# Performance work log

Hardware: AMD Instinct MI355X
Metric: run time of the kernel (lower is better)

## Reference

```python
import jax, jax.numpy as jnp
import numpy as np

N = 50000          # nodes
DEG = 16           # in-degree per node
E = N * DEG        # edges
HID = 128          # hidden_channels (x_channels)
NH = 32            # num_heads (hardcoded in StarPool)
HD = HID // NH     # head dim
ECH = 64           # edge channels = num_rbf + num_edge_attr
NG = 64            # number of graphs in batch
OUT = 1            # output_dim
EPS = 1e-5


def setup_inputs() -> dict:
    key = jax.random.key(0)
    ks = jax.random.split(key, 12)
    x = jax.random.normal(ks[0], (N, HID), jnp.float32)
    edge_attr = jax.random.normal(ks[1], (E, ECH), jnp.float32)
    # edge_index: row0 = source j (random), row1 = target i covering all nodes
    src = jax.random.randint(ks[2], (E,), 0, N, dtype=jnp.int32)
    dst = jnp.repeat(jnp.arange(N, dtype=jnp.int32), DEG)
    edge_index = jnp.stack([src, dst], axis=0)
    batch = jnp.sort(jax.random.randint(ks[3], (N,), 0, NG, dtype=jnp.int32))
    # learned parameters (xavier-ish scaling)
    s_h = 1.0 / np.sqrt(HID)
    s_e = 1.0 / np.sqrt(ECH)
    Wq = jax.random.normal(ks[4], (HID, HID), jnp.float32) * s_h
    bq = jnp.zeros((HID,), jnp.float32)
    Wkv = jax.random.normal(ks[5], (HID, HID), jnp.float32) * s_h
    bkv = jnp.zeros((HID,), jnp.float32)
    Wdk = jax.random.normal(ks[6], (ECH, HID), jnp.float32) * s_e
    bdk = jnp.zeros((HID,), jnp.float32)
    ln_in_g = jnp.ones((HID,), jnp.float32)
    ln_in_b = jnp.zeros((HID,), jnp.float32)
    ln_out_g = jnp.ones((HID,), jnp.float32)
    ln_out_b = jnp.zeros((HID,), jnp.float32)
    Wout = jax.random.normal(ks[7], (HID, OUT), jnp.float32) * s_h
    bout = jnp.zeros((OUT,), jnp.float32)
    return {"x": x, "edge_attr": edge_attr, "Wq": Wq, "bq": bq, "Wkv": Wkv,
            "bkv": bkv, "Wdk": Wdk, "bdk": bdk, "ln_in_g": ln_in_g,
            "ln_in_b": ln_in_b, "ln_out_g": ln_out_g, "ln_out_b": ln_out_b,
            "Wout": Wout, "bout": bout, "edge_index": edge_index, "batch": batch}


def _layernorm(z, g, b):
    m = jnp.mean(z, axis=-1, keepdims=True)
    v = jnp.mean(jnp.square(z - m), axis=-1, keepdims=True)
    return (z - m) * jax.lax.rsqrt(v + EPS) * g + b


def reference(x, edge_attr, Wq, bq, Wkv, bkv, Wdk, bdk,
              ln_in_g, ln_in_b, ln_out_g, ln_out_b, Wout, bout,
              edge_index, batch):
    n = x.shape[0]
    residue = x
    xn = _layernorm(x, ln_in_g, ln_in_b)
    q = (xn @ Wq + bq).reshape(n, NH, HD)
    k = (xn @ Wkv + bkv).reshape(n, NH, HD)          # v = k in StarPool
    dk = (edge_attr @ Wdk + bdk).reshape(-1, NH, HD)
    src, dst = edge_index[0], edge_index[1]          # j (source), i (target)
    k_j = k[src]                                     # [E, NH, HD]
    attn = jax.nn.silu(jnp.sum(q[dst] * k_j * dk, axis=-1))  # [E, NH]
    msg = k_j * attn[:, :, None]                     # [E, NH, HD]
    # scatter-mean over target nodes
    counts = jax.ops.segment_sum(jnp.ones((msg.shape[0],), x.dtype), dst, num_segments=n)
    agg = jax.ops.segment_sum(msg, dst, num_segments=n)
    agg = agg / jnp.clip(counts, 1.0)[:, None, None]
    h = residue + agg.reshape(n, HID)
    # perm = unique(edge_index[1]) == arange(n) by input construction (identity)
    h = residue + _layernorm(h, ln_out_g, ln_out_b)  # dropout p=0 -> identity
    # per-graph mean readout (reduce_op='mean')
    gcnt = jax.ops.segment_sum(jnp.ones((n,), x.dtype), batch, num_segments=NG)
    g = jax.ops.segment_sum(h, batch, num_segments=NG) / jnp.clip(gcnt, 1.0)[:, None]
    # output MLP with 'pass' (identity) activation
    return g @ Wout + bout
```

## Files before the change

### kernel.cpp

```cpp
#include <hip/hip_runtime.h>
#include <hip/hip_bf16.h>

#define N_NODES 50000
#define DEG 16
#define NE 800000
#define HID 128
#define NH 32
#define ECH 64
#define NG 64
#define NSLOT 32
#define LN_EPS 1e-5f

typedef __bf16 bf16x8 __attribute__((ext_vector_type(8)));
typedef float f32x4 __attribute__((ext_vector_type(4)));

__device__ __forceinline__ unsigned short f2bf(float f) {
  unsigned int u = __float_as_uint(f);
  u += 0x7FFFu + ((u >> 16) & 1u);
  return (unsigned short)(u >> 16);
}
__device__ __forceinline__ unsigned int pack2(float a, float b) {
  return (unsigned int)f2bf(a) | ((unsigned int)f2bf(b) << 16);
}

__global__ void prep_kernel(const float* __restrict__ Wq, const float* __restrict__ Wkv,
                            const float* __restrict__ Wdk,
                            unsigned short* __restrict__ WBf,
                            unsigned short* __restrict__ Wdkf,
                            float* __restrict__ gsum) {
  int b = blockIdx.x, t = threadIdx.x;
  if (b < 16) {
    int n = b;
    for (int idx = t; idx < 2048; idx += 256) {
      int j = idx & 7, l = (idx >> 3) & 63, kk = idx >> 9;
      int col = n * 16 + (l & 15);
      int k = kk * 32 + (l >> 4) * 8 + j;
      float v = (col < HID) ? Wq[k * HID + col] : Wkv[k * HID + (col - HID)];
      WBf[((n * 4 + kk) * 64 + l) * 8 + j] = f2bf(v);
    }
  } else if (b < 24) {
    int n2 = b - 16;
    for (int idx = t; idx < 1024; idx += 256) {
      int j = idx & 7, l = (idx >> 3) & 63, kk = idx >> 9;
      int col = n2 * 16 + (l & 15);
      int k = kk * 32 + (l >> 4) * 8 + j;
      Wdkf[((n2 * 2 + kk) * 64 + l) * 8 + j] = f2bf(Wdk[k * HID + col]);
    }
  } else {
    int chunk = b - 24;
    const int tot = NG * NSLOT * HID / 8;
    for (int i = chunk * tot + t; i < (chunk + 1) * tot; i += 256)
      gsum[i] = 0.0f;
  }
}

__global__ __launch_bounds__(256) void node_kernel(
    const float* __restrict__ x, const float* __restrict__ bq,
    const float* __restrict__ bkv, const float* __restrict__ lng,
    const float* __restrict__ lnb, const unsigned short* __restrict__ WBf,
    float* __restrict__ qout, unsigned short* __restrict__ kout) {
  __shared__ __align__(16) unsigned short xn[64 * HID];
  int t = threadIdx.x;
  int node0 = blockIdx.x * 64;
  {
    int row = t >> 2, q4 = t & 3;
    int c0 = q4 * 32;
    int node = node0 + row;
    float v[32];
    if (node < N_NODES) {
      const float4* xp = (const float4*)(x + node * HID + c0);
#pragma unroll
      for (int i = 0; i < 8; i++) {
        float4 f = xp[i];
        v[4 * i] = f.x; v[4 * i + 1] = f.y; v[4 * i + 2] = f.z; v[4 * i + 3] = f.w;
      }
    } else {
#pragma unroll
      for (int i = 0; i < 32; i++) v[i] = 0.f;
    }
    float s = 0.f;
#pragma unroll
    for (int i = 0; i < 32; i++) s += v[i];
    s += __shfl_xor(s, 1); s += __shfl_xor(s, 2);
    float m = s * (1.0f / HID);
    float sq = 0.f;
#pragma unroll
    for (int i = 0; i < 32; i++) { float d = v[i] - m; sq += d * d; }
    sq += __shfl_xor(sq, 1); sq += __shfl_xor(sq, 2);
    float rstd = rsqrtf(sq * (1.0f / HID) + LN_EPS);
#pragma unroll
    for (int ch = 0; ch < 4; ch++) {
      float w0[8];
#pragma unroll
      for (int j = 0; j < 8; j++) {
        int c = c0 + ch * 8 + j;
        w0[j] = (v[ch * 8 + j] - m) * rstd * lng[c] + lnb[c];
      }
      uint4 u;
      u.x = pack2(w0[0], w0[1]); u.y = pack2(w0[2], w0[3]);
      u.z = pack2(w0[4], w0[5]); u.w = pack2(w0[6], w0[7]);
      int byte = row * 256 + ((c0 * 2 + ch * 16) ^ ((row & 7) << 4));
      *(uint4*)((char*)xn + byte) = u;
    }
  }
  __syncthreads();
  int w = t >> 6, l = t & 63;
  int arow = w * 16 + (l & 15);
  bf16x8 a[4];
#pragma unroll
  for (int kk = 0; kk < 4; kk++) {
    int byte = arow * 256 + ((kk * 64 + (l >> 4) * 16) ^ ((arow & 7) << 4));
    a[kk] = *(const bf16x8*)((const char*)xn + byte);
  }
  f32x4 acc[16];
#pragma unroll
  for (int n = 0; n < 16; n++) acc[n] = (f32x4){0.f, 0.f, 0.f, 0.f};
#pragma unroll
  for (int n = 0; n < 16; n++)
#pragma unroll
    for (int kk = 0; kk < 4; kk++) {
      bf16x8 bfr = *(const bf16x8*)(WBf + ((n * 4 + kk) * 64 + l) * 8);
      acc[n] = __builtin_amdgcn_mfma_f32_16x16x32_bf16(a[kk], bfr, acc[n], 0, 0, 0);
    }
#pragma unroll
  for (int n = 0; n < 16; n++) {
    int col = n * 16 + (l & 15);
    float bias = (col < HID) ? bq[col] : bkv[col - HID];
#pragma unroll
    for (int r = 0; r < 4; r++) {
      int node = node0 + w * 16 + (l >> 4) * 4 + r;
      if (node < N_NODES) {
        float vv = acc[n][r] + bias;
        if (col < HID) qout[node * HID + col] = vv;
        else kout[node * HID + (col - HID)] = f2bf(vv);
      }
    }
  }
}

__global__ __launch_bounds__(256, 4) void edge_kernel(
    const float* __restrict__ x, const float* __restrict__ ea,
    const int* __restrict__ src_arr, const int* __restrict__ batch,
    const float* __restrict__ bdk, const float* __restrict__ lng,
    const float* __restrict__ lnb, const float* __restrict__ qg,
    const unsigned short* __restrict__ kbf,
    const unsigned short* __restrict__ Wdkf, float* __restrict__ gsum) {
  __shared__ __align__(16) float xq_s[8 * HID];
  __shared__ __align__(16) float prm_s[3 * HID];
  __shared__ __align__(16) float at_s[4 * 16 * 33];
  __shared__ __align__(16) float h_s[4 * 132];
  __shared__ __align__(16) unsigned short k_s[4 * 16 * HID];
  __shared__ int src_s[64];
  __shared__ int b4[4];
  int t = threadIdx.x;
  int node0 = blockIdx.x * 4;
  int w = t >> 6, l = t & 63, el = l & 15, eh = l >> 4;
  size_t e0n = (size_t)(node0 + w) * DEG;

  xq_s[t]       = x[(size_t)node0 * HID + t];
  xq_s[256 + t] = x[(size_t)node0 * HID + 256 + t];
  xq_s[512 + t] = qg[(size_t)node0 * HID + t];
  xq_s[768 + t] = qg[(size_t)node0 * HID + 256 + t];
  if (t < HID) { prm_s[t] = bdk[t]; prm_s[HID + t] = lng[t]; prm_s[2 * HID + t] = lnb[t]; }
  if (t < 64) src_s[t] = src_arr[(size_t)node0 * DEG + t];
  if (t < 4) b4[t] = batch[node0 + t];

  const float* earow = ea + (e0n + el) * ECH + eh * 8;
  f32x4 ea00 = __builtin_nontemporal_load((const f32x4*)(earow));
  f32x4 ea01 = __builtin_nontemporal_load((const f32x4*)(earow + 4));
  f32x4 ea10 = __builtin_nontemporal_load((const f32x4*)(earow + 32));
  f32x4 ea11 = __builtin_nontemporal_load((const f32x4*)(earow + 36));

  bf16x8 bfr[2];
  bfr[0][0] = (__bf16)ea00[0]; bfr[0][1] = (__bf16)ea00[1];
  bfr[0][2] = (__bf16)ea00[2]; bfr[0][3] = (__bf16)ea00[3];
  bfr[0][4] = (__bf16)ea01[0]; bfr[0][5] = (__bf16)ea01[1];
  bfr[0][6] = (__bf16)ea01[2]; bfr[0][7] = (__bf16)ea01[3];
  bfr[1][0] = (__bf16)ea10[0]; bfr[1][1] = (__bf16)ea10[1];
  bfr[1][2] = (__bf16)ea10[2]; bfr[1][3] = (__bf16)ea10[3];
  bfr[1][4] = (__bf16)ea11[0]; bfr[1][5] = (__bf16)ea11[1];
  bfr[1][6] = (__bf16)ea11[2]; bfr[1][7] = (__bf16)ea11[3];

  __syncthreads();

  unsigned int kw[16];
#pragma unroll
  for (int e = 0; e < 16; e++) {
    int sw = src_s[w * 16 + e];
    kw[e] = *(const unsigned int*)(kbf + (size_t)sw * HID + 2 * l);
  }
  char* kswW = (char*)k_s + w * 4096;
#pragma unroll
  for (int e = 0; e < 16; e++)
    *(unsigned int*)(kswW + e * 256 + ((4 * l) ^ ((e & 7) << 4))) = kw[e];

  f32x4 acc[8];
#pragma unroll
  for (int n = 0; n < 8; n++) acc[n] = (f32x4){0.f, 0.f, 0.f, 0.f};
#pragma unroll
  for (int n = 0; n < 8; n++)
#pragma unroll
    for (int kk = 0; kk < 2; kk++) {
      bf16x8 af = *(const bf16x8*)(Wdkf + ((n * 2 + kk) * 64 + l) * 8);
      acc[n] = __builtin_amdgcn_mfma_f32_16x16x32_bf16(af, bfr[kk], acc[n], 0, 0, 0);
    }

  const char* kswR = (const char*)k_s + w * 4096;
#pragma unroll
  for (int n = 0; n < 8; n++) {
    const int cb = n * 16 + eh * 4;
    f32x4 qv = *(const f32x4*)&xq_s[512 + w * HID + cb];
    f32x4 bd = *(const f32x4*)&prm_s[cb];
    uint2 kk2 = *(const uint2*)(kswR + el * 256 + ((n * 32 + eh * 8) ^ ((el & 7) << 4)));
    float k0 = __uint_as_float(kk2.x << 16);
    float k1 = __uint_as_float(kk2.x & 0xFFFF0000u);
    float k2 = __uint_as_float(kk2.y << 16);
    float k3 = __uint_as_float(kk2.y & 0xFFFF0000u);
    float d0 = acc[n][0] + bd[0];
    float d1 = acc[n][1] + bd[1];
    float d2 = acc[n][2] + bd[2];
    float d3 = acc[n][3] + bd[3];
    float s = qv[0] * k0 * d0 + qv[1] * k1 * d1 + qv[2] * k2 * d2 + qv[3] * k3 * d3;
    float at = s * __builtin_amdgcn_rcpf(1.0f + __expf(-s));
    at_s[w * 528 + el * 33 + n * 4 + eh] = at;
  }

  int hl = l >> 1;
  float macc0 = 0.f, macc1 = 0.f;
#pragma unroll
  for (int e = 0; e < 16; e++) {
    float at = at_s[w * 528 + e * 33 + hl];
    float k0 = __uint_as_float(kw[e] << 16);
    float k1 = __uint_as_float(kw[e] & 0xFFFF0000u);
    macc0 = fmaf(k0, at, macc0);
    macc1 = fmaf(k1, at, macc1);
  }
  float2 xv = *(const float2*)&xq_s[w * HID + 2 * l];
  float h10 = xv.x + macc0 * 0.0625f;
  float h11 = xv.y + macc1 * 0.0625f;
  float ss = h10 + h11;
  ss += __shfl_xor(ss, 1);  ss += __shfl_xor(ss, 2);  ss += __shfl_xor(ss, 4);
  ss += __shfl_xor(ss, 8);  ss += __shfl_xor(ss, 16); ss += __shfl_xor(ss, 32);
  float mean = ss * (1.0f / HID);
  float dv0 = h10 - mean, dv1 = h11 - mean;
  float vv = dv0 * dv0 + dv1 * dv1;
  vv += __shfl_xor(vv, 1);  vv += __shfl_xor(vv, 2);  vv += __shfl_xor(vv, 4);
  vv += __shfl_xor(vv, 8);  vv += __shfl_xor(vv, 16); vv += __shfl_xor(vv, 32);
  float rstd = rsqrtf(vv * (1.0f / HID) + LN_EPS);
  float2 gv = *(const float2*)&prm_s[HID + 2 * l];
  float2 bv = *(const float2*)&prm_s[2 * HID + 2 * l];
  float2 ho;
  ho.x = xv.x + dv0 * rstd * gv.x + bv.x;
  ho.y = xv.y + dv1 * rstd * gv.y + bv.y;
  *(float2*)&h_s[w * 132 + 2 * l] = ho;
  __syncthreads();
  if (t < HID) {
    int c = t;
    int slot = blockIdx.x & (NSLOT - 1);
    float accu = h_s[c];
#pragma unroll
    for (int nn = 1; nn < 4; nn++) {
      if (b4[nn] == b4[nn - 1]) accu += h_s[nn * 132 + c];
      else {
        atomicAdd(&gsum[(b4[nn - 1] * NSLOT + slot) * HID + c], accu);
        accu = h_s[nn * 132 + c];
      }
    }
    atomicAdd(&gsum[(b4[3] * NSLOT + slot) * HID + c], accu);
  }
}

__global__ void readout_kernel(const float* __restrict__ gsum,
                               const int* __restrict__ batch,
                               const float* __restrict__ Wout,
                               const float* __restrict__ bout,
                               float* __restrict__ out) {
  int g = blockIdx.x, l = threadIdx.x;
  int lo = 0, hi = N_NODES;
  while (lo < hi) { int mid = (lo + hi) >> 1; if (batch[mid] < g) lo = mid + 1; else hi = mid; }
  int lo2 = lo, hi2 = N_NODES;
  while (lo2 < hi2) { int mid = (lo2 + hi2) >> 1; if (batch[mid] < g + 1) lo2 = mid + 1; else hi2 = mid; }
  int cnt = lo2 - lo; if (cnt < 1) cnt = 1;
  float a0 = 0.f, a1 = 0.f;
#pragma unroll 4
  for (int s = 0; s < NSLOT; s++) {
    const float* row = gsum + ((size_t)g * NSLOT + s) * HID;
    a0 += row[l];
    a1 += row[64 + l];
  }
  float v = a0 * Wout[l] + a1 * Wout[64 + l];
#pragma unroll
  for (int s = 32; s >= 1; s >>= 1) v += __shfl_xor(v, s);
  if (l == 0) out[g] = v / (float)cnt + bout[0];
}

extern "C" void kernel_launch(void* const* d_in, const int* in_sizes, int n_in,
                              void* d_out, int out_size, void* d_ws, size_t ws_size,
                              hipStream_t stream) {
  const float* x         = (const float*)d_in[0];
  const float* edge_attr = (const float*)d_in[1];
  const float* Wq        = (const float*)d_in[2];
  const float* bq        = (const float*)d_in[3];
  const float* Wkv       = (const float*)d_in[4];
  const float* bkv       = (const float*)d_in[5];
  const float* Wdk       = (const float*)d_in[6];
  const float* bdk       = (const float*)d_in[7];
  const float* ln_in_g   = (const float*)d_in[8];
  const float* ln_in_b   = (const float*)d_in[9];
  const float* ln_out_g  = (const float*)d_in[10];
  const float* ln_out_b  = (const float*)d_in[11];
  const float* Wout      = (const float*)d_in[12];
  const float* bout      = (const float*)d_in[13];
  const int* edge_index  = (const int*)d_in[14];
  const int* batch       = (const int*)d_in[15];
  float* outp = (float*)d_out;

  char* ws = (char*)d_ws;
  float* qbuf          = (float*)ws;
  unsigned short* kbuf = (unsigned short*)(ws + 25600000);
  unsigned short* WBf  = (unsigned short*)(ws + 25600000 + 12800000);
  unsigned short* Wdkf = (unsigned short*)(ws + 25600000 + 12800000 + 65536);
  float* gsum          = (float*)(ws + 25600000 + 12800000 + 65536 + 16384);

  prep_kernel<<<32, 256, 0, stream>>>(Wq, Wkv, Wdk, WBf, Wdkf, gsum);
  node_kernel<<<(N_NODES + 63) / 64, 256, 0, stream>>>(x, bq, bkv, ln_in_g, ln_in_b,
                                                       WBf, qbuf, kbuf);
  edge_kernel<<<N_NODES / 4, 256, 0, stream>>>(x, edge_attr, edge_index, batch, bdk,
                                               ln_out_g, ln_out_b, qbuf, kbuf, Wdkf, gsum);
  readout_kernel<<<NG, 64, 0, stream>>>(gsum, batch, Wout, bout, outp);
}
```

Baseline: 135.3 us.

## Make edge kernel loop over node groups with register double-buffered prefetch

Each edge-kernel block now processes five consecutive 4-node groups in a loop instead of one. While the current group computes, the next group's k-row gather, edge attributes, x/q rows and batch ids are prefetched into a second register buffer, which is meant to hide the latency of the dependent gather. The Wdk fragments are staged once per block in shared memory rather than re-read from global memory by every group. Per-graph partial sums are carried across iterations, so fewer atomics are issued. In exchange, launch bounds drop from 4 to 2 blocks per SIMD to make room for the larger register footprint, which lowers occupancy, and the grid shrinks fivefold.

```diff
diff --git a/kernel.cpp b/kernel.cpp
--- a/kernel.cpp
+++ b/kernel.cpp
@@ -9,6 +9,7 @@
 #define ECH 64
 #define NG 64
 #define NSLOT 32
+#define ITER 5
 #define LN_EPS 1e-5f
 
 typedef __bf16 bf16x8 __attribute__((ext_vector_type(8)));
@@ -138,136 +139,167 @@
   }
 }
 
-__global__ __launch_bounds__(256, 4) void edge_kernel(
+__global__ __launch_bounds__(256, 2) void edge_kernel(
     const float* __restrict__ x, const float* __restrict__ ea,
     const int* __restrict__ src_arr, const int* __restrict__ batch,
     const float* __restrict__ bdk, const float* __restrict__ lng,
     const float* __restrict__ lnb, const float* __restrict__ qg,
     const unsigned short* __restrict__ kbf,
     const unsigned short* __restrict__ Wdkf, float* __restrict__ gsum) {
+  __shared__ __align__(16) unsigned short wdk_s[8 * 2 * 64 * 8];
   __shared__ __align__(16) float xq_s[8 * HID];
   __shared__ __align__(16) float prm_s[3 * HID];
   __shared__ __align__(16) float at_s[4 * 16 * 33];
   __shared__ __align__(16) float h_s[4 * 132];
   __shared__ __align__(16) unsigned short k_s[4 * 16 * HID];
-  __shared__ int src_s[64];
-  __shared__ int b4[4];
+  __shared__ int b4_s[2][4];
   int t = threadIdx.x;
-  int node0 = blockIdx.x * 4;
   int w = t >> 6, l = t & 63, el = l & 15, eh = l >> 4;
-  size_t e0n = (size_t)(node0 + w) * DEG;
-
-  xq_s[t]       = x[(size_t)node0 * HID + t];
-  xq_s[256 + t] = x[(size_t)node0 * HID + 256 + t];
-  xq_s[512 + t] = qg[(size_t)node0 * HID + t];
-  xq_s[768 + t] = qg[(size_t)node0 * HID + 256 + t];
+  int g0 = blockIdx.x * ITER;
+
   if (t < HID) { prm_s[t] = bdk[t]; prm_s[HID + t] = lng[t]; prm_s[2 * HID + t] = lnb[t]; }
-  if (t < 64) src_s[t] = src_arr[(size_t)node0 * DEG + t];
-  if (t < 4) b4[t] = batch[node0 + t];
-
-  const float* earow = ea + (e0n + el) * ECH + eh * 8;
-  f32x4 ea00 = __builtin_nontemporal_load((const f32x4*)(earow));
-  f32x4 ea01 = __builtin_nontemporal_load((const f32x4*)(earow + 4));
-  f32x4 ea10 = __builtin_nontemporal_load((const f32x4*)(earow + 32));
-  f32x4 ea11 = __builtin_nontemporal_load((const f32x4*)(earow + 36));
-
-  bf16x8 bfr[2];
-  bfr[0][0] = (__bf16)ea00[0]; bfr[0][1] = (__bf16)ea00[1];
-  bfr[0][2] = (__bf16)ea00[2]; bfr[0][3] = (__bf16)ea00[3];
-  bfr[0][4] = (__bf16)ea01[0]; bfr[0][5] = (__bf16)ea01[1];
-  bfr[0][6] = (__bf16)ea01[2]; bfr[0][7] = (__bf16)ea01[3];
-  bfr[1][0] = (__bf16)ea10[0]; bfr[1][1] = (__bf16)ea10[1];
-  bfr[1][2] = (__bf16)ea10[2]; bfr[1][3] = (__bf16)ea10[3];
-  bfr[1][4] = (__bf16)ea11[0]; bfr[1][5] = (__bf16)ea11[1];
-  bfr[1][6] = (__bf16)ea11[2]; bfr[1][7] = (__bf16)ea11[3];
-
-  __syncthreads();
-
-  unsigned int kw[16];
-#pragma unroll
-  for (int e = 0; e < 16; e++) {
-    int sw = src_s[w * 16 + e];
-    kw[e] = *(const unsigned int*)(kbf + (size_t)sw * HID + 2 * l);
-  }
-  char* kswW = (char*)k_s + w * 4096;
-#pragma unroll
-  for (int e = 0; e < 16; e++)
-    *(unsigned int*)(kswW + e * 256 + ((4 * l) ^ ((e & 7) << 4))) = kw[e];
-
-  f32x4 acc[8];
-#pragma unroll
-  for (int n = 0; n < 8; n++) acc[n] = (f32x4){0.f, 0.f, 0.f, 0.f};
-#pragma unroll
-  for (int n = 0; n < 8; n++)
-#pragma unroll
-    for (int kk = 0; kk < 2; kk++) {
-      bf16x8 af = *(const bf16x8*)(Wdkf + ((n * 2 + kk) * 64 + l) * 8);
-      acc[n] = __builtin_amdgcn_mfma_f32_16x16x32_bf16(af, bfr[kk], acc[n], 0, 0, 0);
-    }
-
-  const char* kswR = (const char*)k_s + w * 4096;
-#pragma unroll
-  for (int n = 0; n < 8; n++) {
-    const int cb = n * 16 + eh * 4;
-    f32x4 qv = *(const f32x4*)&xq_s[512 + w * HID + cb];
-    f32x4 bd = *(const f32x4*)&prm_s[cb];
-    uint2 kk2 = *(const uint2*)(kswR + el * 256 + ((n * 32 + eh * 8) ^ ((el & 7) << 4)));
-    float k0 = __uint_as_float(kk2.x << 16);
-    float k1 = __uint_as_float(kk2.x & 0xFFFF0000u);
-    float k2 = __uint_as_float(kk2.y << 16);
-    float k3 = __uint_as_float(kk2.y & 0xFFFF0000u);
-    float d0 = acc[n][0] + bd[0];
-    float d1 = acc[n][1] + bd[1];
-    float d2 = acc[n][2] + bd[2];
-    float d3 = acc[n][3] + bd[3];
-    float s = qv[0] * k0 * d0 + qv[1] * k1 * d1 + qv[2] * k2 * d2 + qv[3] * k3 * d3;
-    float at = s * __builtin_amdgcn_rcpf(1.0f + __expf(-s));
-    at_s[w * 528 + el * 33 + n * 4 + eh] = at;
-  }
-
-  int hl = l >> 1;
-  float macc0 = 0.f, macc1 = 0.f;
-#pragma unroll
-  for (int e = 0; e < 16; e++) {
-    float at = at_s[w * 528 + e * 33 + hl];
-    float k0 = __uint_as_float(kw[e] << 16);
-    float k1 = __uint_as_float(kw[e] & 0xFFFF0000u);
-    macc0 = fmaf(k0, at, macc0);
-    macc1 = fmaf(k1, at, macc1);
-  }
-  float2 xv = *(const float2*)&xq_s[w * HID + 2 * l];
-  float h10 = xv.x + macc0 * 0.0625f;
-  float h11 = xv.y + macc1 * 0.0625f;
-  float ss = h10 + h11;
-  ss += __shfl_xor(ss, 1);  ss += __shfl_xor(ss, 2);  ss += __shfl_xor(ss, 4);
-  ss += __shfl_xor(ss, 8);  ss += __shfl_xor(ss, 16); ss += __shfl_xor(ss, 32);
-  float mean = ss * (1.0f / HID);
-  float dv0 = h10 - mean, dv1 = h11 - mean;
-  float vv = dv0 * dv0 + dv1 * dv1;
-  vv += __shfl_xor(vv, 1);  vv += __shfl_xor(vv, 2);  vv += __shfl_xor(vv, 4);
-  vv += __shfl_xor(vv, 8);  vv += __shfl_xor(vv, 16); vv += __shfl_xor(vv, 32);
-  float rstd = rsqrtf(vv * (1.0f / HID) + LN_EPS);
-  float2 gv = *(const float2*)&prm_s[HID + 2 * l];
-  float2 bv = *(const float2*)&prm_s[2 * HID + 2 * l];
-  float2 ho;
-  ho.x = xv.x + dv0 * rstd * gv.x + bv.x;
-  ho.y = xv.y + dv1 * rstd * gv.y + bv.y;
-  *(float2*)&h_s[w * 132 + 2 * l] = ho;
-  __syncthreads();
-  if (t < HID) {
-    int c = t;
-    int slot = blockIdx.x & (NSLOT - 1);
-    float accu = h_s[c];
-#pragma unroll
-    for (int nn = 1; nn < 4; nn++) {
-      if (b4[nn] == b4[nn - 1]) accu += h_s[nn * 132 + c];
-      else {
-        atomicAdd(&gsum[(b4[nn - 1] * NSLOT + slot) * HID + c], accu);
-        accu = h_s[nn * 132 + c];
-      }
-    }
-    atomicAdd(&gsum[(b4[3] * NSLOT + slot) * HID + c], accu);
-  }
+#pragma unroll
+  for (int i = 0; i < 4; i++) {
+    int idx = (i * 256 + t) * 8;
+    *(uint4*)(wdk_s + idx) = *(const uint4*)(Wdkf + idx);
+  }
+
+  int slot = blockIdx.x & (NSLOT - 1);
+  int curG = batch[g0 * 4];
+  float accu = 0.f;
+
+  unsigned int kwR[2][16];
+  f32x4 eaR[2][4];
+  float xqR[2][4];
+  int srcR[2], b4R[2];
+
+  auto LOAD_SRC = [&](int g) -> int {
+    return src_arr[(size_t)g * 64 + w * 16 + el];
+  };
+  auto LOAD_GROUP = [&](int g, int s) {
+    size_t node0 = (size_t)g * 4;
+    const float* earow = ea + ((node0 + w) * DEG + el) * ECH + eh * 8;
+    eaR[s][0] = __builtin_nontemporal_load((const f32x4*)(earow));
+    eaR[s][1] = __builtin_nontemporal_load((const f32x4*)(earow + 4));
+    eaR[s][2] = __builtin_nontemporal_load((const f32x4*)(earow + 32));
+    eaR[s][3] = __builtin_nontemporal_load((const f32x4*)(earow + 36));
+    xqR[s][0] = x[node0 * HID + t];
+    xqR[s][1] = x[node0 * HID + 256 + t];
+    xqR[s][2] = qg[node0 * HID + t];
+    xqR[s][3] = qg[node0 * HID + 256 + t];
+    b4R[s] = batch[node0 + (t & 3)];
+  };
+  auto GATHER = [&](int s) {
+    int sv = srcR[s];
+#pragma unroll
+    for (int e = 0; e < 16; e++) {
+      int sw = __shfl(sv, e, 16);
+      kwR[s][e] = *(const unsigned int*)(kbf + (size_t)sw * HID + 2 * l);
+    }
+  };
+
+  srcR[0] = LOAD_SRC(g0);
+  LOAD_GROUP(g0, 0);
+  srcR[1] = LOAD_SRC(g0 + 1);
+  GATHER(0);
+
+#pragma unroll
+  for (int i = 0; i < ITER; i++) {
+    const int cur = i & 1, nxt = cur ^ 1;
+    if (i + 1 < ITER) GATHER(nxt);
+    if (i + 2 < ITER) srcR[cur] = LOAD_SRC(g0 + i + 2);
+    if (i + 1 < ITER) LOAD_GROUP(g0 + i + 1, nxt);
+    xq_s[t]       = xqR[cur][0];
+    xq_s[256 + t] = xqR[cur][1];
+    xq_s[512 + t] = xqR[cur][2];
+    xq_s[768 + t] = xqR[cur][3];
+    if (t < 4) b4_s[cur][t] = b4R[cur];
+    __syncthreads();
+    bf16x8 bfr[2];
+#pragma unroll
+    for (int kk = 0; kk < 2; kk++)
+#pragma unroll
+      for (int j = 0; j < 4; j++) {
+        bfr[kk][j]     = (__bf16)eaR[cur][kk * 2][j];
+        bfr[kk][4 + j] = (__bf16)eaR[cur][kk * 2 + 1][j];
+      }
+    char* kswW = (char*)k_s + w * 4096;
+#pragma unroll
+    for (int e = 0; e < 16; e++)
+      *(unsigned int*)(kswW + e * 256 + ((4 * l) ^ ((e & 7) << 4))) = kwR[cur][e];
+    f32x4 acc[8];
+#pragma unroll
+    for (int n = 0; n < 8; n++) acc[n] = (f32x4){0.f, 0.f, 0.f, 0.f};
+#pragma unroll
+    for (int n = 0; n < 8; n++)
+#pragma unroll
+      for (int kk = 0; kk < 2; kk++) {
+        bf16x8 af = *(const bf16x8*)(wdk_s + ((n * 2 + kk) * 64 + l) * 8);
+        acc[n] = __builtin_amdgcn_mfma_f32_16x16x32_bf16(af, bfr[kk], acc[n], 0, 0, 0);
+      }
+    const char* kswR = (const char*)k_s + w * 4096;
+#pragma unroll
+    for (int n = 0; n < 8; n++) {
+      const int cb = n * 16 + eh * 4;
+      f32x4 qv = *(const f32x4*)&xq_s[512 + w * HID + cb];
+      f32x4 bd = *(const f32x4*)&prm_s[cb];
+      uint2 kk2 = *(const uint2*)(kswR + el * 256 + ((n * 32 + eh * 8) ^ ((el & 7) << 4)));
+      float k0 = __uint_as_float(kk2.x << 16);
+      float k1 = __uint_as_float(kk2.x & 0xFFFF0000u);
+      float k2 = __uint_as_float(kk2.y << 16);
+      float k3 = __uint_as_float(kk2.y & 0xFFFF0000u);
+      float d0 = acc[n][0] + bd[0];
+      float d1 = acc[n][1] + bd[1];
+      float d2 = acc[n][2] + bd[2];
+      float d3 = acc[n][3] + bd[3];
+      float s = qv[0] * k0 * d0 + qv[1] * k1 * d1 + qv[2] * k2 * d2 + qv[3] * k3 * d3;
+      float at = s * __builtin_amdgcn_rcpf(1.0f + __expf(-s));
+      at_s[w * 528 + el * 33 + n * 4 + eh] = at;
+    }
+    int hl = l >> 1;
+    float macc0 = 0.f, macc1 = 0.f;
+#pragma unroll
+    for (int e = 0; e < 16; e++) {
+      float at = at_s[w * 528 + e * 33 + hl];
+      float k0 = __uint_as_float(kwR[cur][e] << 16);
+      float k1 = __uint_as_float(kwR[cur][e] & 0xFFFF0000u);
+      macc0 = fmaf(k0, at, macc0);
+      macc1 = fmaf(k1, at, macc1);
+    }
+    float2 xv = *(const float2*)&xq_s[w * HID + 2 * l];
+    float h10 = xv.x + macc0 * 0.0625f;
+    float h11 = xv.y + macc1 * 0.0625f;
+    float ss = h10 + h11;
+    ss += __shfl_xor(ss, 1);  ss += __shfl_xor(ss, 2);  ss += __shfl_xor(ss, 4);
+    ss += __shfl_xor(ss, 8);  ss += __shfl_xor(ss, 16); ss += __shfl_xor(ss, 32);
+    float mean = ss * (1.0f / HID);
+    float dv0 = h10 - mean, dv1 = h11 - mean;
+    float vv = dv0 * dv0 + dv1 * dv1;
+    vv += __shfl_xor(vv, 1);  vv += __shfl_xor(vv, 2);  vv += __shfl_xor(vv, 4);
+    vv += __shfl_xor(vv, 8);  vv += __shfl_xor(vv, 16); vv += __shfl_xor(vv, 32);
+    float rstd = rsqrtf(vv * (1.0f / HID) + LN_EPS);
+    float2 gv = *(const float2*)&prm_s[HID + 2 * l];
+    float2 bv = *(const float2*)&prm_s[2 * HID + 2 * l];
+    float2 ho;
+    ho.x = xv.x + dv0 * rstd * gv.x + bv.x;
+    ho.y = xv.y + dv1 * rstd * gv.y + bv.y;
+    *(float2*)&h_s[w * 132 + 2 * l] = ho;
+    __syncthreads();
+    if (t < HID) {
+#pragma unroll
+      for (int nn = 0; nn < 4; nn++) {
+        int gph = b4_s[cur][nn];
+        if (gph != curG) {
+          atomicAdd(&gsum[(curG * NSLOT + slot) * HID + t], accu);
+          accu = 0.f;
+          curG = gph;
+        }
+        accu += h_s[nn * 132 + t];
+      }
+    }
+  }
+  if (t < HID)
+    atomicAdd(&gsum[(curG * NSLOT + slot) * HID + t], accu);
 }
 
 __global__ void readout_kernel(const float* __restrict__ gsum,
@@ -325,7 +357,8 @@
   prep_kernel<<<32, 256, 0, stream>>>(Wq, Wkv, Wdk, WBf, Wdkf, gsum);
   node_kernel<<<(N_NODES + 63) / 64, 256, 0, stream>>>(x, bq, bkv, ln_in_g, ln_in_b,
                                                        WBf, qbuf, kbuf);
-  edge_kernel<<<N_NODES / 4, 256, 0, stream>>>(x, edge_attr, edge_index, batch, bdk,
-                                               ln_out_g, ln_out_b, qbuf, kbuf, Wdkf, gsum);
+  edge_kernel<<<N_NODES / 4 / ITER, 256, 0, stream>>>(x, edge_attr, edge_index, batch,
+                                                      bdk, ln_out_g, ln_out_b, qbuf,
+                                                      kbuf, Wdkf, gsum);
   readout_kernel<<<NG, 64, 0, stream>>>(gsum, batch, Wout, bout, outp);
 }
```

Measured after the change: 126.4 us. -6.6%, faster.

## Make edge kernel persistent per wave with software-pipelined prefetch of next node

Applied to the files above, without the earlier changes.

Each wave now handles ITER consecutive nodes instead of one. While computing the current node it prefetches the next node's gathered K rows, edge attributes, x row, batch id and source indices, keeping the Wdk fragments in registers across iterations. Block-level shared staging and the two __syncthreads are removed, and graph-sum atomics are accumulated per wave and flushed only when the batch id changes. This aims to hide gather latency and amortise weight loads and atomics, but register pressure rises and launch bounds drop to 3 waves per SIMD, which lowers occupancy.

```diff
diff --git a/kernel.cpp b/kernel.cpp
--- a/kernel.cpp
+++ b/kernel.cpp
@@ -9,6 +9,7 @@
 #define ECH 64
 #define NG 64
 #define NSLOT 32
+#define ITER 5
 #define LN_EPS 1e-5f
 
 typedef __bf16 bf16x8 __attribute__((ext_vector_type(8)));
@@ -138,136 +139,146 @@
   }
 }
 
-__global__ __launch_bounds__(256, 4) void edge_kernel(
+__global__ __launch_bounds__(256, 3) void edge_kernel(
     const float* __restrict__ x, const float* __restrict__ ea,
     const int* __restrict__ src_arr, const int* __restrict__ batch,
     const float* __restrict__ bdk, const float* __restrict__ lng,
     const float* __restrict__ lnb, const float* __restrict__ qg,
     const unsigned short* __restrict__ kbf,
     const unsigned short* __restrict__ Wdkf, float* __restrict__ gsum) {
-  __shared__ __align__(16) float xq_s[8 * HID];
-  __shared__ __align__(16) float prm_s[3 * HID];
-  __shared__ __align__(16) float at_s[4 * 16 * 33];
-  __shared__ __align__(16) float h_s[4 * 132];
-  __shared__ __align__(16) unsigned short k_s[4 * 16 * HID];
-  __shared__ int src_s[64];
-  __shared__ int b4[4];
-  int t = threadIdx.x;
-  int node0 = blockIdx.x * 4;
-  int w = t >> 6, l = t & 63, el = l & 15, eh = l >> 4;
-  size_t e0n = (size_t)(node0 + w) * DEG;
-
-  xq_s[t]       = x[(size_t)node0 * HID + t];
-  xq_s[256 + t] = x[(size_t)node0 * HID + 256 + t];
-  xq_s[512 + t] = qg[(size_t)node0 * HID + t];
-  xq_s[768 + t] = qg[(size_t)node0 * HID + 256 + t];
-  if (t < HID) { prm_s[t] = bdk[t]; prm_s[HID + t] = lng[t]; prm_s[2 * HID + t] = lnb[t]; }
-  if (t < 64) src_s[t] = src_arr[(size_t)node0 * DEG + t];
-  if (t < 4) b4[t] = batch[node0 + t];
-
-  const float* earow = ea + (e0n + el) * ECH + eh * 8;
-  f32x4 ea00 = __builtin_nontemporal_load((const f32x4*)(earow));
-  f32x4 ea01 = __builtin_nontemporal_load((const f32x4*)(earow + 4));
-  f32x4 ea10 = __builtin_nontemporal_load((const f32x4*)(earow + 32));
-  f32x4 ea11 = __builtin_nontemporal_load((const f32x4*)(earow + 36));
-
-  bf16x8 bfr[2];
-  bfr[0][0] = (__bf16)ea00[0]; bfr[0][1] = (__bf16)ea00[1];
-  bfr[0][2] = (__bf16)ea00[2]; bfr[0][3] = (__bf16)ea00[3];
-  bfr[0][4] = (__bf16)ea01[0]; bfr[0][5] = (__bf16)ea01[1];
-  bfr[0][6] = (__bf16)ea01[2]; bfr[0][7] = (__bf16)ea01[3];
-  bfr[1][0] = (__bf16)ea10[0]; bfr[1][1] = (__bf16)ea10[1];
-  bfr[1][2] = (__bf16)ea10[2]; bfr[1][3] = (__bf16)ea10[3];
-  bfr[1][4] = (__bf16)ea11[0]; bfr[1][5] = (__bf16)ea11[1];
-  bfr[1][6] = (__bf16)ea11[2]; bfr[1][7] = (__bf16)ea11[3];
-
-  __syncthreads();
+  __shared__ __align__(16) unsigned short k_s[4][2048];
+  __shared__ __align__(16) float at_s[4][16 * 33];
+  int t = threadIdx.x, w = t >> 6, l = t & 63, el = l & 15, eh = l >> 4;
+  int wslot = blockIdx.x * 4 + w;
+  int n0 = wslot * ITER;
+  int slot = wslot & (NSLOT - 1);
+  char* ksw = (char*)&k_s[w][0];
+  float* atw = &at_s[w][0];
+
+  bf16x8 wdkR[16];
+#pragma unroll
+  for (int j = 0; j < 16; j++)
+    wdkR[j] = *(const bf16x8*)(Wdkf + (j * 64 + l) * 8);
+
+  int curG = batch[n0];
+  float accu0 = 0.f, accu1 = 0.f;
 
   unsigned int kw[16];
+  f32x4 eaR[4];
+  float2 xvN;
+  int srcA, srcB, bN;
+
+  srcA = src_arr[(size_t)n0 * DEG + el];
+  {
+    const float* p = ea + ((size_t)n0 * DEG + el) * ECH + eh * 8;
+    eaR[0] = __builtin_nontemporal_load((const f32x4*)p);
+    eaR[1] = __builtin_nontemporal_load((const f32x4*)(p + 4));
+    eaR[2] = __builtin_nontemporal_load((const f32x4*)(p + 32));
+    eaR[3] = __builtin_nontemporal_load((const f32x4*)(p + 36));
+  }
+  xvN = *(const float2*)(x + (size_t)n0 * HID + 2 * l);
+  bN = curG;
+  srcB = (ITER > 1) ? src_arr[(size_t)(n0 + 1) * DEG + el] : 0;
 #pragma unroll
   for (int e = 0; e < 16; e++) {
-    int sw = src_s[w * 16 + e];
+    int sw = __shfl(srcA, e, 16);
     kw[e] = *(const unsigned int*)(kbf + (size_t)sw * HID + 2 * l);
   }
-  char* kswW = (char*)k_s + w * 4096;
-#pragma unroll
-  for (int e = 0; e < 16; e++)
-    *(unsigned int*)(kswW + e * 256 + ((4 * l) ^ ((e & 7) << 4))) = kw[e];
-
-  f32x4 acc[8];
-#pragma unroll
-  for (int n = 0; n < 8; n++) acc[n] = (f32x4){0.f, 0.f, 0.f, 0.f};
-#pragma unroll
-  for (int n = 0; n < 8; n++)
-#pragma unroll
-    for (int kk = 0; kk < 2; kk++) {
-      bf16x8 af = *(const bf16x8*)(Wdkf + ((n * 2 + kk) * 64 + l) * 8);
-      acc[n] = __builtin_amdgcn_mfma_f32_16x16x32_bf16(af, bfr[kk], acc[n], 0, 0, 0);
-    }
-
-  const char* kswR = (const char*)k_s + w * 4096;
-#pragma unroll
-  for (int n = 0; n < 8; n++) {
-    const int cb = n * 16 + eh * 4;
-    f32x4 qv = *(const f32x4*)&xq_s[512 + w * HID + cb];
-    f32x4 bd = *(const f32x4*)&prm_s[cb];
-    uint2 kk2 = *(const uint2*)(kswR + el * 256 + ((n * 32 + eh * 8) ^ ((el & 7) << 4)));
-    float k0 = __uint_as_float(kk2.x << 16);
-    float k1 = __uint_as_float(kk2.x & 0xFFFF0000u);
-    float k2 = __uint_as_float(kk2.y << 16);
-    float k3 = __uint_as_float(kk2.y & 0xFFFF0000u);
-    float d0 = acc[n][0] + bd[0];
-    float d1 = acc[n][1] + bd[1];
-    float d2 = acc[n][2] + bd[2];
-    float d3 = acc[n][3] + bd[3];
-    float s = qv[0] * k0 * d0 + qv[1] * k1 * d1 + qv[2] * k2 * d2 + qv[3] * k3 * d3;
-    float at = s * __builtin_amdgcn_rcpf(1.0f + __expf(-s));
-    at_s[w * 528 + el * 33 + n * 4 + eh] = at;
-  }
-
-  int hl = l >> 1;
-  float macc0 = 0.f, macc1 = 0.f;
-#pragma unroll
-  for (int e = 0; e < 16; e++) {
-    float at = at_s[w * 528 + e * 33 + hl];
-    float k0 = __uint_as_float(kw[e] << 16);
-    float k1 = __uint_as_float(kw[e] & 0xFFFF0000u);
-    macc0 = fmaf(k0, at, macc0);
-    macc1 = fmaf(k1, at, macc1);
-  }
-  float2 xv = *(const float2*)&xq_s[w * HID + 2 * l];
-  float h10 = xv.x + macc0 * 0.0625f;
-  float h11 = xv.y + macc1 * 0.0625f;
-  float ss = h10 + h11;
-  ss += __shfl_xor(ss, 1);  ss += __shfl_xor(ss, 2);  ss += __shfl_xor(ss, 4);
-  ss += __shfl_xor(ss, 8);  ss += __shfl_xor(ss, 16); ss += __shfl_xor(ss, 32);
-  float mean = ss * (1.0f / HID);
-  float dv0 = h10 - mean, dv1 = h11 - mean;
-  float vv = dv0 * dv0 + dv1 * dv1;
-  vv += __shfl_xor(vv, 1);  vv += __shfl_xor(vv, 2);  vv += __shfl_xor(vv, 4);
-  vv += __shfl_xor(vv, 8);  vv += __shfl_xor(vv, 16); vv += __shfl_xor(vv, 32);
-  float rstd = rsqrtf(vv * (1.0f / HID) + LN_EPS);
-  float2 gv = *(const float2*)&prm_s[HID + 2 * l];
-  float2 bv = *(const float2*)&prm_s[2 * HID + 2 * l];
-  float2 ho;
-  ho.x = xv.x + dv0 * rstd * gv.x + bv.x;
-  ho.y = xv.y + dv1 * rstd * gv.y + bv.y;
-  *(float2*)&h_s[w * 132 + 2 * l] = ho;
-  __syncthreads();
-  if (t < HID) {
-    int c = t;
-    int slot = blockIdx.x & (NSLOT - 1);
-    float accu = h_s[c];
-#pragma unroll
-    for (int nn = 1; nn < 4; nn++) {
-      if (b4[nn] == b4[nn - 1]) accu += h_s[nn * 132 + c];
-      else {
-        atomicAdd(&gsum[(b4[nn - 1] * NSLOT + slot) * HID + c], accu);
-        accu = h_s[nn * 132 + c];
-      }
-    }
-    atomicAdd(&gsum[(b4[3] * NSLOT + slot) * HID + c], accu);
-  }
+
+#pragma unroll
+  for (int i = 0; i < ITER; i++) {
+    const int ni = n0 + i;
+#pragma unroll
+    for (int e = 0; e < 16; e++)
+      *(unsigned int*)(ksw + e * 256 + ((4 * l) ^ ((e & 7) << 4))) = kw[e];
+    bf16x8 bfr[2];
+#pragma unroll
+    for (int kk = 0; kk < 2; kk++)
+#pragma unroll
+      for (int j = 0; j < 4; j++) {
+        bfr[kk][j]     = (__bf16)eaR[kk * 2][j];
+        bfr[kk][4 + j] = (__bf16)eaR[kk * 2 + 1][j];
+      }
+    float2 xv = xvN;
+    int b_cur = bN;
+    if (i + 1 < ITER) {
+#pragma unroll
+      for (int e = 0; e < 16; e++) {
+        int sw = __shfl(srcB, e, 16);
+        kw[e] = *(const unsigned int*)(kbf + (size_t)sw * HID + 2 * l);
+      }
+      const float* p = ea + ((size_t)(ni + 1) * DEG + el) * ECH + eh * 8;
+      eaR[0] = __builtin_nontemporal_load((const f32x4*)p);
+      eaR[1] = __builtin_nontemporal_load((const f32x4*)(p + 4));
+      eaR[2] = __builtin_nontemporal_load((const f32x4*)(p + 32));
+      eaR[3] = __builtin_nontemporal_load((const f32x4*)(p + 36));
+      xvN = *(const float2*)(x + (size_t)(ni + 1) * HID + 2 * l);
+      bN = batch[ni + 1];
+    }
+    if (i + 2 < ITER) srcB = src_arr[(size_t)(ni + 2) * DEG + el];
+#pragma unroll
+    for (int half = 0; half < 2; half++) {
+      f32x4 acc[4];
+#pragma unroll
+      for (int n4 = 0; n4 < 4; n4++) {
+        int n = half * 4 + n4;
+        acc[n4] = *(const f32x4*)(bdk + n * 16 + eh * 4);
+      }
+#pragma unroll
+      for (int n4 = 0; n4 < 4; n4++) {
+        int n = half * 4 + n4;
+        acc[n4] = __builtin_amdgcn_mfma_f32_16x16x32_bf16(wdkR[n * 2], bfr[0], acc[n4], 0, 0, 0);
+        acc[n4] = __builtin_amdgcn_mfma_f32_16x16x32_bf16(wdkR[n * 2 + 1], bfr[1], acc[n4], 0, 0, 0);
+      }
+#pragma unroll
+      for (int n4 = 0; n4 < 4; n4++) {
+        int n = half * 4 + n4;
+        const int cb = n * 16 + eh * 4;
+        f32x4 qv = *(const f32x4*)(qg + (size_t)ni * HID + cb);
+        uint2 kk2 = *(const uint2*)(ksw + el * 256 + ((n * 32 + eh * 8) ^ ((el & 7) << 4)));
+        float k0 = __uint_as_float(kk2.x << 16);
+        float k1 = __uint_as_float(kk2.x & 0xFFFF0000u);
+        float k2 = __uint_as_float(kk2.y << 16);
+        float k3 = __uint_as_float(kk2.y & 0xFFFF0000u);
+        float s = qv[0] * k0 * acc[n4][0] + qv[1] * k1 * acc[n4][1]
+                + qv[2] * k2 * acc[n4][2] + qv[3] * k3 * acc[n4][3];
+        float at = s * __builtin_amdgcn_rcpf(1.0f + __expf(-s));
+        atw[el * 33 + n * 4 + eh] = at;
+      }
+    }
+    int hl = l >> 1;
+    float m0 = 0.f, m1 = 0.f;
+#pragma unroll
+    for (int e = 0; e < 16; e++) {
+      float at = atw[e * 33 + hl];
+      unsigned int kv = *(const unsigned int*)(ksw + e * 256 + ((4 * l) ^ ((e & 7) << 4)));
+      m0 = fmaf(__uint_as_float(kv << 16), at, m0);
+      m1 = fmaf(__uint_as_float(kv & 0xFFFF0000u), at, m1);
+    }
+    float h10 = xv.x + m0 * 0.0625f;
+    float h11 = xv.y + m1 * 0.0625f;
+    float ss = h10 + h11;
+    ss += __shfl_xor(ss, 1);  ss += __shfl_xor(ss, 2);  ss += __shfl_xor(ss, 4);
+    ss += __shfl_xor(ss, 8);  ss += __shfl_xor(ss, 16); ss += __shfl_xor(ss, 32);
+    float mean = ss * (1.0f / HID);
+    float dv0 = h10 - mean, dv1 = h11 - mean;
+    float vv = dv0 * dv0 + dv1 * dv1;
+    vv += __shfl_xor(vv, 1);  vv += __shfl_xor(vv, 2);  vv += __shfl_xor(vv, 4);
+    vv += __shfl_xor(vv, 8);  vv += __shfl_xor(vv, 16); vv += __shfl_xor(vv, 32);
+    float rstd = rsqrtf(vv * (1.0f / HID) + LN_EPS);
+    float2 gv = *(const float2*)(lng + 2 * l);
+    float2 bv = *(const float2*)(lnb + 2 * l);
+    float ho0 = xv.x + dv0 * rstd * gv.x + bv.x;
+    float ho1 = xv.y + dv1 * rstd * gv.y + bv.y;
+    if (b_cur != curG) {
+      atomicAdd(&gsum[(curG * NSLOT + slot) * HID + 2 * l], accu0);
+      atomicAdd(&gsum[(curG * NSLOT + slot) * HID + 2 * l + 1], accu1);
+      accu0 = 0.f; accu1 = 0.f; curG = b_cur;
+    }
+    accu0 += ho0; accu1 += ho1;
+  }
+  atomicAdd(&gsum[(curG * NSLOT + slot) * HID + 2 * l], accu0);
+  atomicAdd(&gsum[(curG * NSLOT + slot) * HID + 2 * l + 1], accu1);
 }
 
 __global__ void readout_kernel(const float* __restrict__ gsum,
@@ -325,7 +336,8 @@
   prep_kernel<<<32, 256, 0, stream>>>(Wq, Wkv, Wdk, WBf, Wdkf, gsum);
   node_kernel<<<(N_NODES + 63) / 64, 256, 0, stream>>>(x, bq, bkv, ln_in_g, ln_in_b,
                                                        WBf, qbuf, kbuf);
-  edge_kernel<<<N_NODES / 4, 256, 0, stream>>>(x, edge_attr, edge_index, batch, bdk,
-                                               ln_out_g, ln_out_b, qbuf, kbuf, Wdkf, gsum);
+  edge_kernel<<<N_NODES / (4 * ITER), 256, 0, stream>>>(x, edge_attr, edge_index, batch,
+                                                        bdk, ln_out_g, ln_out_b, qbuf,
+                                                        kbuf, Wdkf, gsum);
   readout_kernel<<<NG, 64, 0, stream>>>(gsum, batch, Wout, bout, outp);
 }
```

Result: slower. 177.7 us (+31.3%).
